# Kernel optimization log

Measured on AMD Instinct MI355X. Metric: run time of the kernel, lower is better.

## Reference

```python
import jax, jax.numpy as jnp
import numpy as np

HEADS = 8
DIM_HEAD = 64
DIM = 512
HIDDEN = HEADS * DIM_HEAD  # 512


def setup_inputs() -> dict:
    key = jax.random.key(0)
    k1, k2, k3, k4 = jax.random.split(key, 4)
    B, H, W = 8, 64, 64
    x = jax.random.normal(k1, (B, DIM, H, W), dtype=jnp.float32)
    # Conv2d 1x1 weights stored as [out_ch, in_ch] (kernel 1x1 squeezed)
    w_qkv = jax.random.normal(k2, (3 * HIDDEN, DIM), dtype=jnp.float32) * (1.0 / np.sqrt(DIM))
    w_out = jax.random.normal(k3, (DIM, HIDDEN), dtype=jnp.float32) * (1.0 / np.sqrt(HIDDEN))
    b_out = jax.random.normal(k4, (DIM,), dtype=jnp.float32) * 0.01
    return {"x": x, "w_qkv": w_qkv, "w_out": w_out, "b_out": b_out}


def reference(x, w_qkv, w_out, b_out):
    b, c, h, w = x.shape
    n = h * w
    # to_qkv: 1x1 conv == channel GEMM
    qkv = jnp.einsum('bchw,oc->bohw', x, w_qkv)               # [b, 3*heads*dh, h, w]
    qkv = qkv.reshape(b, 3, HEADS, DIM_HEAD, n)               # split (qkv heads c), flatten (h w)
    q, k, v = qkv[:, 0], qkv[:, 1], qkv[:, 2]                 # each [b, heads, dh, n]
    k = jax.nn.softmax(k, axis=-1)                            # softmax over spatial tokens
    context = jnp.einsum('bhdn,bhen->bhde', k, v)             # [b, heads, dh, dh]
    out = jnp.einsum('bhde,bhdn->bhen', context, q)           # [b, heads, dh, n]
    out = out.reshape(b, HIDDEN, h, w)
    # to_out: 1x1 conv with bias
    return jnp.einsum('bchw,oc->bohw', out, w_out) + b_out[None, :, None, None]
```

## Files before the change

kernel.cpp:

```cpp
#include <hip/hip_runtime.h>
#include <hip/hip_bf16.h>


typedef __attribute__((ext_vector_type(8))) __bf16 bf16x8;
typedef __attribute__((ext_vector_type(4))) float f32x4;
typedef __attribute__((ext_vector_type(8))) unsigned short u16x8;
typedef __attribute__((ext_vector_type(4))) float float4v;

__device__ __forceinline__ unsigned short f2b(float f) {
  unsigned int u = __builtin_bit_cast(unsigned int, f);
  unsigned int r = (u + 0x7FFFu + ((u >> 16) & 1u)) >> 16;
  return (unsigned short)r;
}
__device__ __forceinline__ float b2f(unsigned short h) {
  unsigned int u = ((unsigned int)h) << 16;
  return __builtin_bit_cast(float, u);
}

__global__ __launch_bounds__(256) void prep_wkv_kernel(const float* __restrict__ w,
                                                       unsigned short* __restrict__ wkv) {
  int i = (blockIdx.x * 256 + threadIdx.x) * 4;
  const float* src = w + 512 * 512;
  #pragma unroll
  for (int j = 0; j < 4; ++j) wkv[i + j] = f2b(src[i + j]);
}

__global__ __launch_bounds__(256) void prep_wqT_kernel(const float* __restrict__ w,
                                                       unsigned short* __restrict__ WqT) {
  __shared__ unsigned short tile[64][65];
  const int ct = blockIdx.x, ot = blockIdx.y;
  const int c0 = ct * 64, o0 = ot * 64;
  const int tc = threadIdx.x & 63, tr = threadIdx.x >> 6;
  #pragma unroll
  for (int i = 0; i < 16; ++i) {
    int row = tr * 16 + i;
    tile[tc][row] = f2b(w[(long)(o0 + row) * 512 + c0 + tc]);
  }
  __syncthreads();
  #pragma unroll
  for (int i = 0; i < 16; ++i) {
    int row = tr * 16 + i;
    WqT[(long)(c0 + row) * 512 + o0 + tc] = tile[row][tc];
  }
}

__global__ __launch_bounds__(256) void transpose_x_kernel(const float* __restrict__ x,
                                                          unsigned short* __restrict__ xT) {
  __shared__ unsigned short tile[64][65];
  const int b = blockIdx.z, ct = blockIdx.y, nt = blockIdx.x;
  const int c0 = ct * 64, n0 = nt * 64;
  const int tid = threadIdx.x;

  const int n_off = (tid & 15) * 4;
  const float* xp = x + ((long)b * 512) * 4096 + n0;
  #pragma unroll
  for (int i = 0; i < 4; ++i) {
    int c_local = i * 16 + (tid >> 4);
    float4v v = *(const float4v*)(xp + (long)(c0 + c_local) * 4096 + n_off);
    #pragma unroll
    for (int j = 0; j < 4; ++j) tile[n_off + j][c_local] = f2b(v[j]);
  }
  __syncthreads();

  const int n_row = tid >> 2;
  const int c_seg = (tid & 3) * 16;
  unsigned short* xtp = xT + ((long)b * 4096 + n0 + n_row) * 512 + c0 + c_seg;
  #pragma unroll
  for (int s = 0; s < 2; ++s) {
    u16x8 o;
    #pragma unroll
    for (int k = 0; k < 8; ++k) o[k] = tile[n_row][c_seg + s * 8 + k];
    *(u16x8*)(xtp + s * 8) = o;
  }
}

__global__ __launch_bounds__(256) void gemm128_bt(
    const unsigned short* __restrict__ A, long strideA,
    const unsigned short* __restrict__ BT, long strideBT,
    void* __restrict__ Cout, long strideC, int ldc,
    const float* __restrict__ bias) {
  constexpr int K = 512;
  const int b = blockIdx.z;
  const int m0 = blockIdx.y * 128;
  const int n0 = blockIdx.x * 128;
  const unsigned short* Ab = A + (long)b * strideA;
  const unsigned short* Bb = BT + (long)b * strideBT;

  __shared__ unsigned short lds[2 * 128 * 64];
  char* ldsc = (char*)lds;

  const int tid = threadIdx.x;
  const int wave = tid >> 6;
  const int lane = tid & 63;
  const int wr = wave >> 1;
  const int wc = wave & 1;

  f32x4 acc[4][4];
  const f32x4 zero = {0.f, 0.f, 0.f, 0.f};
  #pragma unroll
  for (int i = 0; i < 4; ++i)
    #pragma unroll
    for (int j = 0; j < 4; ++j) acc[i][j] = zero;

  for (int kt = 0; kt < K; kt += 64) {
    #pragma unroll
    for (int q = 0; q < 4; ++q) {
      unsigned base = q * 4096 + wave * 1024;
      unsigned D = base + lane * 16;
      unsigned row = D >> 7;
      unsigned g = (D >> 4) & 7;
      unsigned gl = g ^ (row & 7);
      const unsigned short* srcA = Ab + (long)(m0 + row) * K + kt + gl * 8;
      __builtin_amdgcn_global_load_lds(
          (const __attribute__((address_space(1))) unsigned int*)srcA,
          (__attribute__((address_space(3))) unsigned int*)(ldsc + base), 16, 0, 0);
      const unsigned short* srcB = Bb + (long)(n0 + row) * K + kt + gl * 8;
      __builtin_amdgcn_global_load_lds(
          (const __attribute__((address_space(1))) unsigned int*)srcB,
          (__attribute__((address_space(3))) unsigned int*)(ldsc + 16384 + base), 16, 0, 0);
    }
    __syncthreads();

    bf16x8 af[2][4], bfr[2][4];
    #pragma unroll
    for (int ks = 0; ks < 2; ++ks) {
      #pragma unroll
      for (int mi = 0; mi < 4; ++mi) {
        unsigned row = wr * 64 + mi * 16 + (lane & 15);
        unsigned g = ((unsigned)(ks * 4 + (lane >> 4))) ^ (row & 7);
        af[ks][mi] = *(const bf16x8*)(ldsc + row * 128 + g * 16);
      }
      #pragma unroll
      for (int ni = 0; ni < 4; ++ni) {
        unsigned row = wc * 64 + ni * 16 + (lane & 15);
        unsigned g = ((unsigned)(ks * 4 + (lane >> 4))) ^ (row & 7);
        bfr[ks][ni] = *(const bf16x8*)(ldsc + 16384 + row * 128 + g * 16);
      }
    }
    #pragma unroll
    for (int ks = 0; ks < 2; ++ks)
      #pragma unroll
      for (int mi = 0; mi < 4; ++mi)
        #pragma unroll
        for (int ni = 0; ni < 4; ++ni)
          acc[mi][ni] = __builtin_amdgcn_mfma_f32_16x16x32_bf16(
              af[ks][mi], bfr[ks][ni], acc[mi][ni], 0, 0, 0);
    __syncthreads();
  }

  const int r0 = (lane >> 4) * 4;
  const int cn = lane & 15;
  if (bias != nullptr) {
    float* C = (float*)Cout + (long)b * strideC;
    #pragma unroll
    for (int mi = 0; mi < 4; ++mi) {
      int o = m0 + wr * 64 + mi * 16 + r0;
      #pragma unroll
      for (int ni = 0; ni < 4; ++ni) {
        int n = n0 + wc * 64 + ni * 16 + cn;
        #pragma unroll
        for (int r = 0; r < 4; ++r)
          C[(long)(o + r) * ldc + n] = acc[mi][ni][r] + bias[o + r];
      }
    }
  } else {
    unsigned short* C = (unsigned short*)Cout + (long)b * strideC;
    #pragma unroll
    for (int mi = 0; mi < 4; ++mi) {
      int o = m0 + wr * 64 + mi * 16 + r0;
      #pragma unroll
      for (int ni = 0; ni < 4; ++ni) {
        int n = n0 + wc * 64 + ni * 16 + cn;
        #pragma unroll
        for (int r = 0; r < 4; ++r)
          C[(long)(o + r) * ldc + n] = f2b(acc[mi][ni][r]);
      }
    }
  }
}

__global__ __launch_bounds__(256) void gemm64_bt(
    const unsigned short* __restrict__ A, long strideA,
    const unsigned short* __restrict__ BT, long strideBT,
    void* __restrict__ Cout, long strideC, int ldc,
    const float* __restrict__ bias) {
  constexpr int K = 512;
  const int b = blockIdx.z;
  const int m0 = blockIdx.y * 64;
  const int n0 = blockIdx.x * 128;
  const unsigned short* Ab = A + (long)b * strideA;
  const unsigned short* Bb = BT + (long)b * strideBT;

  __shared__ unsigned short lds[(64 + 128) * 64];
  char* ldsc = (char*)lds;

  const int tid = threadIdx.x;
  const int wave = tid >> 6;
  const int lane = tid & 63;
  const int wc = wave;

  f32x4 acc[4][2];
  const f32x4 zero = {0.f, 0.f, 0.f, 0.f};
  #pragma unroll
  for (int i = 0; i < 4; ++i)
    #pragma unroll
    for (int j = 0; j < 2; ++j) acc[i][j] = zero;

  for (int kt = 0; kt < K; kt += 64) {
    #pragma unroll
    for (int q = 0; q < 2; ++q) {
      unsigned base = q * 4096 + wave * 1024;
      unsigned D = base + lane * 16;
      unsigned row = D >> 7;
      unsigned g = (D >> 4) & 7;
      unsigned gl = g ^ (row & 7);
      const unsigned short* srcA = Ab + (long)(m0 + row) * K + kt + gl * 8;
      __builtin_amdgcn_global_load_lds(
          (const __attribute__((address_space(1))) unsigned int*)srcA,
          (__attribute__((address_space(3))) unsigned int*)(ldsc + base), 16, 0, 0);
    }
    #pragma unroll
    for (int q = 0; q < 4; ++q) {
      unsigned base = q * 4096 + wave * 1024;
      unsigned D = base + lane * 16;
      unsigned row = D >> 7;
      unsigned g = (D >> 4) & 7;
      unsigned gl = g ^ (row & 7);
      const unsigned short* srcB = Bb + (long)(n0 + row) * K + kt + gl * 8;
      __builtin_amdgcn_global_load_lds(
          (const __attribute__((address_space(1))) unsigned int*)srcB,
          (__attribute__((address_space(3))) unsigned int*)(ldsc + 8192 + base), 16, 0, 0);
    }
    __syncthreads();

    bf16x8 af[2][4], bfr[2][2];
    #pragma unroll
    for (int ks = 0; ks < 2; ++ks) {
      #pragma unroll
      for (int mi = 0; mi < 4; ++mi) {
        unsigned row = mi * 16 + (lane & 15);
        unsigned g = ((unsigned)(ks * 4 + (lane >> 4))) ^ (row & 7);
        af[ks][mi] = *(const bf16x8*)(ldsc + row * 128 + g * 16);
      }
      #pragma unroll
      for (int ni = 0; ni < 2; ++ni) {
        unsigned row = wc * 32 + ni * 16 + (lane & 15);
        unsigned g = ((unsigned)(ks * 4 + (lane >> 4))) ^ (row & 7);
        bfr[ks][ni] = *(const bf16x8*)(ldsc + 8192 + row * 128 + g * 16);
      }
    }
    #pragma unroll
    for (int ks = 0; ks < 2; ++ks)
      #pragma unroll
      for (int mi = 0; mi < 4; ++mi)
        #pragma unroll
        for (int ni = 0; ni < 2; ++ni)
          acc[mi][ni] = __builtin_amdgcn_mfma_f32_16x16x32_bf16(
              af[ks][mi], bfr[ks][ni], acc[mi][ni], 0, 0, 0);
    __syncthreads();
  }

  const int r0 = (lane >> 4) * 4;
  const int cn = lane & 15;
  if (bias != nullptr) {
    float* C = (float*)Cout + (long)b * strideC;
    #pragma unroll
    for (int mi = 0; mi < 4; ++mi) {
      int o = m0 + mi * 16 + r0;
      #pragma unroll
      for (int ni = 0; ni < 2; ++ni) {
        int n = n0 + wc * 32 + ni * 16 + cn;
        #pragma unroll
        for (int r = 0; r < 4; ++r)
          C[(long)(o + r) * ldc + n] = acc[mi][ni][r] + bias[o + r];
      }
    }
  } else {
    unsigned short* C = (unsigned short*)Cout + (long)b * strideC;
    #pragma unroll
    for (int mi = 0; mi < 4; ++mi) {
      int o = m0 + mi * 16 + r0;
      #pragma unroll
      for (int ni = 0; ni < 2; ++ni) {
        int n = n0 + wc * 32 + ni * 16 + cn;
        #pragma unroll
        for (int r = 0; r < 4; ++r)
          C[(long)(o + r) * ldc + n] = f2b(acc[mi][ni][r]);
      }
    }
  }
}

__global__ __launch_bounds__(256) void context_full_kernel(const unsigned short* __restrict__ kv,
                                                           float* __restrict__ ctx) {
  const int bh = blockIdx.x, b = bh >> 3, h = bh & 7;
  const unsigned short* Kp = kv + ((long)b * 1024 + h * 64) * 4096;
  const unsigned short* Vp = kv + ((long)b * 1024 + 512 + h * 64) * 4096;
  const int tid = threadIdx.x, wave = tid >> 6, lane = tid & 63;

  __shared__ float sm[64], ss[64];

  {
    const int r = tid >> 2, sub = tid & 3;
    const unsigned short* rp = Kp + (long)r * 4096 + sub * 8;
    float m = -3.4e38f, s = 0.f;
    #pragma unroll 4
    for (int j = 0; j < 128; ++j) {
      u16x8 v8 = *(const u16x8*)(rp + j * 32);
      float v[8];
      #pragma unroll
      for (int i = 0; i < 8; ++i) v[i] = b2f(v8[i]);
      float vm = fmaxf(fmaxf(fmaxf(v[0], v[1]), fmaxf(v[2], v[3])),
                       fmaxf(fmaxf(v[4], v[5]), fmaxf(v[6], v[7])));
      if (vm > m) { s *= __expf(m - vm); m = vm; }
      #pragma unroll
      for (int i = 0; i < 8; ++i) s += __expf(v[i] - m);
    }
    #pragma unroll
    for (int off = 1; off <= 2; off <<= 1) {
      float mo = __shfl_xor(m, off);
      float so = __shfl_xor(s, off);
      float mn = fmaxf(m, mo);
      s = s * __expf(m - mn) + so * __expf(mo - mn);
      m = mn;
    }
    if (sub == 0) { sm[r] = m; ss[r] = 1.0f / s; }
  }
  __syncthreads();

  float mrow[4], srow[4];
  #pragma unroll
  for (int mi = 0; mi < 4; ++mi) {
    int rA = mi * 16 + (lane & 15);
    mrow[mi] = sm[rA];
    srow[mi] = ss[rA];
  }

  f32x4 acc[4][4];
  const f32x4 zero = {0.f, 0.f, 0.f, 0.f};
  #pragma unroll
  for (int i = 0; i < 4; ++i)
    #pragma unroll
    for (int j = 0; j < 4; ++j) acc[i][j] = zero;

  const int kbeg = wave * 1024;
  for (int k0 = kbeg; k0 < kbeg + 1024; k0 += 32) {
    const int kc = k0 + (lane >> 4) * 8;
    bf16x8 a[4], bv[4];
    #pragma unroll
    for (int mi = 0; mi < 4; ++mi) {
      u16x8 kr = *(const u16x8*)(Kp + (long)(mi * 16 + (lane & 15)) * 4096 + kc);
      u16x8 pr;
      #pragma unroll
      for (int j = 0; j < 8; ++j)
        pr[j] = f2b(__expf(b2f(kr[j]) - mrow[mi]) * srow[mi]);
      a[mi] = __builtin_bit_cast(bf16x8, pr);
    }
    #pragma unroll
    for (int ni = 0; ni < 4; ++ni)
      bv[ni] = *(const bf16x8*)(Vp + (long)(ni * 16 + (lane & 15)) * 4096 + kc);
    #pragma unroll
    for (int mi = 0; mi < 4; ++mi)
      #pragma unroll
      for (int ni = 0; ni < 4; ++ni)
        acc[mi][ni] = __builtin_amdgcn_mfma_f32_16x16x32_bf16(a[mi], bv[ni], acc[mi][ni], 0, 0, 0);
  }

  __shared__ float part[4][64][64];
  #pragma unroll
  for (int mi = 0; mi < 4; ++mi)
    #pragma unroll
    for (int ni = 0; ni < 4; ++ni)
      #pragma unroll
      for (int r = 0; r < 4; ++r)
        part[wave][mi * 16 + (lane >> 4) * 4 + r][ni * 16 + (lane & 15)] = acc[mi][ni][r];
  __syncthreads();
  float* cp = ctx + (long)bh * 4096;
  for (int i = tid; i < 4096; i += 256) {
    int dd = i >> 6, ee = i & 63;
    cp[i] = part[0][dd][ee] + part[1][dd][ee] + part[2][dd][ee] + part[3][dd][ee];
  }
}

__global__ __launch_bounds__(256) void w2_kernel(const float* __restrict__ ctx,
                                                 const float* __restrict__ w_out,
                                                 unsigned short* __restrict__ W2) {
  const int cq = blockIdx.x, bh = blockIdx.y, b = bh >> 3, h = bh & 7;
  __shared__ float cs[64][65];
  const int tid = threadIdx.x;
  for (int i = tid; i < 4096; i += 256) cs[i >> 6][i & 63] = ctx[(long)bh * 4096 + i];
  __syncthreads();
  const int c = cq * 128 + (tid & 127);
  const int dbeg = (tid >> 7) * 32;
  const float* wp = w_out + (long)c * 512 + h * 64;
  float wrow[64];
  #pragma unroll
  for (int e = 0; e < 64; ++e) wrow[e] = wp[e];
  unsigned short* W2p = W2 + ((long)b * 512 + c) * 512 + h * 64;
  for (int dd = dbeg; dd < dbeg + 32; ++dd) {
    float s = 0.f;
    #pragma unroll
    for (int e = 0; e < 64; ++e) s = fmaf(wrow[e], cs[dd][e], s);
    W2p[dd] = f2b(s);
  }
}

extern "C" void kernel_launch(void* const* d_in, const int* in_sizes, int n_in,
                              void* d_out, int out_size, void* d_ws, size_t ws_size,
                              hipStream_t stream) {
  const float* x     = (const float*)d_in[0];
  const float* w_qkv = (const float*)d_in[1];
  const float* w_out = (const float*)d_in[2];
  const float* b_out = (const float*)d_in[3];

  char* ws = (char*)d_ws;
  unsigned short* xT   = (unsigned short*)ws;
  unsigned short* kv   = (unsigned short*)(ws + 33554432);
  unsigned short* wkv  = (unsigned short*)(ws + 100663296);
  unsigned short* WqT  = (unsigned short*)(ws + 101711872);
  float*          ctx  = (float*)(ws + 102268928);
  unsigned short* W2   = (unsigned short*)(ws + 110657536);
  unsigned short* W3   = (unsigned short*)(ws + 114851840);

  prep_wkv_kernel<<<dim3(512), dim3(256), 0, stream>>>(w_qkv, wkv);
  prep_wqT_kernel<<<dim3(8, 8), dim3(256), 0, stream>>>(w_qkv, WqT);
  transpose_x_kernel<<<dim3(64, 8, 8), dim3(256), 0, stream>>>(x, xT);
  gemm128_bt<<<dim3(32, 8, 8), dim3(256), 0, stream>>>(
      wkv, 0L, xT, (long)4096 * 512, (void*)kv, (long)1024 * 4096, 4096, (const float*)nullptr);
  context_full_kernel<<<dim3(64), dim3(256), 0, stream>>>(kv, ctx);
  w2_kernel<<<dim3(4, 64), dim3(256), 0, stream>>>(ctx, w_out, W2);
  gemm64_bt<<<dim3(4, 8, 8), dim3(256), 0, stream>>>(
      W2, (long)512 * 512, WqT, 0L, (void*)W3, (long)512 * 512, 512, (const float*)nullptr);
  gemm64_bt<<<dim3(32, 8, 8), dim3(256), 0, stream>>>(
      W3, (long)512 * 512, xT, (long)4096 * 512, d_out, (long)512 * 4096, 4096, b_out);
}
```

Measured before the change: 193.1 us.

## Split softmax stats and context into separate kernels with split-K over tokens

The single 64-block context kernel, which computed softmax row statistics and the K·V context serially per head, is split in two. A 4096-block rowstat kernel computes each key row's max and inverse sum, and a context kernel launched with 8 token slices per head writes partial contexts that w2_kernel sums. This exposes far more parallelism on a GPU with many CUs, in exchange for an extra launch, an extra read of K, and 8x partial-context traffic.

```diff
diff --git a/kernel.cpp b/kernel.cpp
--- a/kernel.cpp
+++ b/kernel.cpp
@@ -291,49 +291,58 @@
   }
 }
 
-__global__ __launch_bounds__(256) void context_full_kernel(const unsigned short* __restrict__ kv,
-                                                           float* __restrict__ ctx) {
-  const int bh = blockIdx.x, b = bh >> 3, h = bh & 7;
+__global__ __launch_bounds__(256) void rowstat_kernel(const unsigned short* __restrict__ kv,
+                                                      float* __restrict__ stats) {
+  const int row = blockIdx.x;
+  const int b = row >> 9, d = row & 511;
+  const unsigned short* kp = kv + ((long)b * 1024 + d) * 4096;
+  const int tid = threadIdx.x, wave = tid >> 6, lane = tid & 63;
+  __shared__ float red[8];
+
+  float v[16];
+  u16x8 l0 = *(const u16x8*)(kp + tid * 8);
+  u16x8 l1 = *(const u16x8*)(kp + 2048 + tid * 8);
+  #pragma unroll
+  for (int j = 0; j < 8; ++j) { v[j] = b2f(l0[j]); v[8 + j] = b2f(l1[j]); }
+
+  float m = v[0];
+  #pragma unroll
+  for (int j = 1; j < 16; ++j) m = fmaxf(m, v[j]);
+  #pragma unroll
+  for (int off = 32; off > 0; off >>= 1) m = fmaxf(m, __shfl_xor(m, off));
+  if (lane == 0) red[wave] = m;
+  __syncthreads();
+  m = fmaxf(fmaxf(red[0], red[1]), fmaxf(red[2], red[3]));
+
+  float s = 0.f;
+  #pragma unroll
+  for (int j = 0; j < 16; ++j) s += __expf(v[j] - m);
+  #pragma unroll
+  for (int off = 32; off > 0; off >>= 1) s += __shfl_xor(s, off);
+  if (lane == 0) red[4 + wave] = s;
+  __syncthreads();
+  if (tid == 0) {
+    s = red[4] + red[5] + red[6] + red[7];
+    stats[2 * row] = m;
+    stats[2 * row + 1] = 1.0f / s;
+  }
+}
+
+__global__ __launch_bounds__(256) void context_kernel(const unsigned short* __restrict__ kv,
+                                                      const float* __restrict__ stats,
+                                                      float* __restrict__ ctx_part) {
+  const int s = blockIdx.x, bh = blockIdx.y, b = bh >> 3, h = bh & 7;
   const unsigned short* Kp = kv + ((long)b * 1024 + h * 64) * 4096;
   const unsigned short* Vp = kv + ((long)b * 1024 + 512 + h * 64) * 4096;
+  const float* sb = stats + ((long)b * 512 + h * 64) * 2;
   const int tid = threadIdx.x, wave = tid >> 6, lane = tid & 63;
-
-  __shared__ float sm[64], ss[64];
-
-  {
-    const int r = tid >> 2, sub = tid & 3;
-    const unsigned short* rp = Kp + (long)r * 4096 + sub * 8;
-    float m = -3.4e38f, s = 0.f;
-    #pragma unroll 4
-    for (int j = 0; j < 128; ++j) {
-      u16x8 v8 = *(const u16x8*)(rp + j * 32);
-      float v[8];
-      #pragma unroll
-      for (int i = 0; i < 8; ++i) v[i] = b2f(v8[i]);
-      float vm = fmaxf(fmaxf(fmaxf(v[0], v[1]), fmaxf(v[2], v[3])),
-                       fmaxf(fmaxf(v[4], v[5]), fmaxf(v[6], v[7])));
-      if (vm > m) { s *= __expf(m - vm); m = vm; }
-      #pragma unroll
-      for (int i = 0; i < 8; ++i) s += __expf(v[i] - m);
-    }
-    #pragma unroll
-    for (int off = 1; off <= 2; off <<= 1) {
-      float mo = __shfl_xor(m, off);
-      float so = __shfl_xor(s, off);
-      float mn = fmaxf(m, mo);
-      s = s * __expf(m - mn) + so * __expf(mo - mn);
-      m = mn;
-    }
-    if (sub == 0) { sm[r] = m; ss[r] = 1.0f / s; }
-  }
-  __syncthreads();
 
   float mrow[4], srow[4];
   #pragma unroll
   for (int mi = 0; mi < 4; ++mi) {
     int rA = mi * 16 + (lane & 15);
-    mrow[mi] = sm[rA];
-    srow[mi] = ss[rA];
+    mrow[mi] = sb[2 * rA];
+    srow[mi] = sb[2 * rA + 1];
   }
 
   f32x4 acc[4][4];
@@ -343,8 +352,8 @@
     #pragma unroll
     for (int j = 0; j < 4; ++j) acc[i][j] = zero;
 
-  const int kbeg = wave * 1024;
-  for (int k0 = kbeg; k0 < kbeg + 1024; k0 += 32) {
+  const int kbeg = s * 512 + wave * 128;
+  for (int k0 = kbeg; k0 < kbeg + 128; k0 += 32) {
     const int kc = k0 + (lane >> 4) * 8;
     bf16x8 a[4], bv[4];
     #pragma unroll
@@ -375,20 +384,25 @@
       for (int r = 0; r < 4; ++r)
         part[wave][mi * 16 + (lane >> 4) * 4 + r][ni * 16 + (lane & 15)] = acc[mi][ni][r];
   __syncthreads();
-  float* cp = ctx + (long)bh * 4096;
+  float* cp = ctx_part + ((long)(s * 64 + bh)) * 4096;
   for (int i = tid; i < 4096; i += 256) {
     int dd = i >> 6, ee = i & 63;
     cp[i] = part[0][dd][ee] + part[1][dd][ee] + part[2][dd][ee] + part[3][dd][ee];
   }
 }
 
-__global__ __launch_bounds__(256) void w2_kernel(const float* __restrict__ ctx,
+__global__ __launch_bounds__(256) void w2_kernel(const float* __restrict__ ctx_part,
                                                  const float* __restrict__ w_out,
                                                  unsigned short* __restrict__ W2) {
   const int cq = blockIdx.x, bh = blockIdx.y, b = bh >> 3, h = bh & 7;
   __shared__ float cs[64][65];
   const int tid = threadIdx.x;
-  for (int i = tid; i < 4096; i += 256) cs[i >> 6][i & 63] = ctx[(long)bh * 4096 + i];
+  for (int i = tid; i < 4096; i += 256) {
+    float v = 0.f;
+    #pragma unroll
+    for (int s = 0; s < 8; ++s) v += ctx_part[((long)(s * 64 + bh)) * 4096 + i];
+    cs[i >> 6][i & 63] = v;
+  }
   __syncthreads();
   const int c = cq * 128 + (tid & 127);
   const int dbeg = (tid >> 7) * 32;
@@ -418,7 +432,8 @@
   unsigned short* kv   = (unsigned short*)(ws + 33554432);
   unsigned short* wkv  = (unsigned short*)(ws + 100663296);
   unsigned short* WqT  = (unsigned short*)(ws + 101711872);
-  float*          ctx  = (float*)(ws + 102268928);
+  float*          stats= (float*)(ws + 102236160);
+  float*          ctxp = (float*)(ws + 102268928);
   unsigned short* W2   = (unsigned short*)(ws + 110657536);
   unsigned short* W3   = (unsigned short*)(ws + 114851840);
 
@@ -427,8 +442,9 @@
   transpose_x_kernel<<<dim3(64, 8, 8), dim3(256), 0, stream>>>(x, xT);
   gemm128_bt<<<dim3(32, 8, 8), dim3(256), 0, stream>>>(
       wkv, 0L, xT, (long)4096 * 512, (void*)kv, (long)1024 * 4096, 4096, (const float*)nullptr);
-  context_full_kernel<<<dim3(64), dim3(256), 0, stream>>>(kv, ctx);
-  w2_kernel<<<dim3(4, 64), dim3(256), 0, stream>>>(ctx, w_out, W2);
+  rowstat_kernel<<<dim3(4096), dim3(256), 0, stream>>>(kv, stats);
+  context_kernel<<<dim3(8, 64), dim3(256), 0, stream>>>(kv, stats, ctxp);
+  w2_kernel<<<dim3(4, 64), dim3(256), 0, stream>>>(ctxp, w_out, W2);
   gemm64_bt<<<dim3(4, 8, 8), dim3(256), 0, stream>>>(
       W2, (long)512 * 512, WqT, 0L, (void*)W3, (long)512 * 512, 512, (const float*)nullptr);
   gemm64_bt<<<dim3(32, 8, 8), dim3(256), 0, stream>>>(
```

Result: faster. 167.6 us (-13.2%).
